# Kernel tuning notes

Hardware: AMD Instinct MI355X
Metric: run time of the kernel (lower is better)

The kernel has to match this reference:

```python
import jax, jax.numpy as jnp
import numpy as np


def conv1x1(x, W, b):
    # x: [B,C,H,W], W: [O,C] (1x1 conv kernel squeezed), b: [O]
    return jnp.einsum('bchw,oc->bohw', x, W) + b[None, :, None, None]


def setup_inputs() -> dict:
    key = jax.random.key(0)
    ks = jax.random.split(key, 16)
    B, C, H, W = 4, 2048, 32, 32
    HID = 256  # gate_strength_fc hidden width
    s = 1.0 / np.sqrt(C)
    x = jax.random.normal(ks[0], (B, C, H, W), dtype=jnp.float32)
    mask = jax.random.uniform(ks[1], (B, 1, H, W)) > 0.8
    use_entropy_gate = jax.random.randint(ks[2], (B,), 0, 2).astype(bool)
    return {
        'x': x,
        'Wq': jax.random.normal(ks[3], (C, C)) * s,
        'bq': jnp.zeros((C,), jnp.float32),
        'Wk': jax.random.normal(ks[4], (C, C)) * s,
        'bk': jnp.zeros((C,), jnp.float32),
        'Wv': jax.random.normal(ks[5], (C, C)) * s,
        'bv': jnp.zeros((C,), jnp.float32),
        'Wg': jax.random.normal(ks[6], (C, C)) * s,
        'bg': jnp.zeros((C,), jnp.float32),
        'W1': jax.random.normal(ks[7], (HID, C)) * s,
        'b1': jnp.zeros((HID,), jnp.float32),
        'W2': jax.random.normal(ks[8], (1, HID)) * (1.0 / np.sqrt(HID)),
        'b2': jnp.zeros((1,), jnp.float32),
        'mask': mask,
        'use_entropy_gate': use_entropy_gate,
    }


def reference(x, Wq, bq, Wk, bk, Wv, bv, Wg, bg, W1, b1, W2, b2, mask, use_entropy_gate):
    B, C, H, W = x.shape
    HW = H * W
    masked_x = x * mask.astype(x.dtype)
    # 1x1 conv projections, flattened over spatial dims
    q = conv1x1(masked_x, Wq, bq).reshape(B, C, HW).transpose(0, 2, 1)  # [B,HW,C]
    k = conv1x1(masked_x, Wk, bk).reshape(B, C, HW)                     # [B,C,HW]
    v = conv1x1(x, Wv, bv).reshape(B, C, HW)                            # [B,C,HW]
    # attention[b,n,m] = softmax_m(q[b,n,:] . k[b,:,m])
    attn = jax.nn.softmax(jnp.einsum('bnc,bcm->bnm', q, k), axis=-1)    # [B,HW,HW]
    # out = bmm(value, attention^T): out[b,c,m] = sum_n v[b,c,n] * attn[b,m,n]
    out = jnp.einsum('bcn,bmn->bcm', v, attn).reshape(B, C, H, W)
    # gate strength head: 2048 -> 256 -> 1, then sigmoid
    gate_strength = jax.nn.sigmoid(conv1x1(jax.nn.relu(conv1x1(x, W1, b1)), W2, b2))  # [B,1,H,W]
    gate = jax.nn.sigmoid(conv1x1(x, Wg, bg))                                          # [B,C,H,W]
    gated = out * gate * gate_strength
    # per-sample select: gated attention output where flag set, else passthrough x
    return jnp.where(use_entropy_gate[:, None, None, None], gated, x)
```

## Files before the change

kernel.cpp:

```cpp
#include <hip/hip_runtime.h>
#include <cstddef>
#include <cstdint>


typedef unsigned int u32;
typedef unsigned short u16;
typedef __attribute__((ext_vector_type(8))) short bf16x8;
typedef __attribute__((ext_vector_type(4))) float f32x4;

#define B_   4
#define C_   2048
#define HW_  1024
#define HID_ 256
#define KP   384
#define NQK  384
#define NVGH 1088

__device__ __forceinline__ float sigmoidf_(float x) {
  return 1.0f / (1.0f + __expf(-x));
}
__device__ __forceinline__ u16 f2bf(float f) {
  u32 u = __float_as_uint(f);
  return (u16)((u + 0x7FFFu + ((u >> 16) & 1u)) >> 16);
}
__device__ __forceinline__ float bf2f(u16 h) {
  return __uint_as_float(((u32)h) << 16);
}
__device__ __forceinline__ void gld16(void* lds, const void* g) {
  __builtin_amdgcn_global_load_lds(
      (const __attribute__((address_space(1))) u32*)g,
      (__attribute__((address_space(3))) u32*)lds, 16, 0, 0);
}

__device__ __forceinline__ void stage128x32s(u16* lds, const u16* g, int ld, int tid) {
#pragma unroll
  for (int t = 0; t < 2; ++t) {
    int s = tid + t * 256;
    int row = s >> 2;
    int oct = ((s & 3) - (row >> 1)) & 3;
    gld16(lds + (size_t)s * 8, g + (size_t)row * ld + oct * 8);
  }
}
template <int NF>
__device__ __forceinline__ void read_frags_s(const u16* lds, int base, int ln, int kq,
                                             bf16x8* f) {
#pragma unroll
  for (int t = 0; t < NF; ++t) {
    int row = base + t * 16 + ln;
    int oct = (kq + (row >> 1)) & 3;
    f[t] = *(const bf16x8*)(lds + (size_t)row * 32 + oct * 8);
  }
}

__global__ __launch_bounds__(256)
void scan_mask(const int* __restrict__ mask, int* __restrict__ idx,
               int* __restrict__ rnk, int* __restrict__ cnt)
{
  const int b = blockIdx.x;
  const int t = threadIdx.x;
  __shared__ int base;
  if (t == 0) base = 0;
  __syncthreads();
  int m0 = t * 4;
  int mv[4], local = 0;
#pragma unroll
  for (int i = 0; i < 4; ++i) { mv[i] = mask[b * HW_ + m0 + i] != 0; local += mv[i]; }
  int my = atomicAdd(&base, local);
#pragma unroll
  for (int i = 0; i < 4; ++i) {
    if (mv[i]) {
      int r = my++;
      if (r < KP) { idx[b * KP + r] = m0 + i; rnk[b * HW_ + m0 + i] = r; }
      else rnk[b * HW_ + m0 + i] = -1;
    } else {
      rnk[b * HW_ + m0 + i] = -1;
    }
  }
  __syncthreads();
  if (t == 0) cnt[b] = min(base, KP);
}

__global__ __launch_bounds__(256)
void transpose_fused(const float* __restrict__ x, u16* __restrict__ xhi,
                     u16* __restrict__ xkh, u16* __restrict__ xkl,
                     const int* __restrict__ rnk, const int* __restrict__ useg)
{
  const int b = blockIdx.z;
  if (!useg[b]) return;
  __shared__ float t[32][33];
  const int c0 = blockIdx.y * 32, j0 = blockIdx.x * 32;
  const int tid = threadIdx.x;
  const float* xb = x + ((size_t)b * C_ + c0) * (size_t)HW_ + j0;
  {
    int jj = tid & 31, cs = tid >> 5;
#pragma unroll
    for (int t4 = 0; t4 < 4; ++t4) {
      int c = cs * 4 + t4;
      t[c][jj] = xb[(size_t)c * HW_ + jj];
    }
  }
  __syncthreads();
  int j = tid >> 3, c4 = (tid & 7) * 4;
  float v0 = t[c4 + 0][j], v1 = t[c4 + 1][j], v2 = t[c4 + 2][j], v3 = t[c4 + 3][j];
  ushort4 hv;
  hv.x = f2bf(v0); hv.y = f2bf(v1); hv.z = f2bf(v2); hv.w = f2bf(v3);
  *(ushort4*)(xhi + ((size_t)b * HW_ + j0 + j) * (size_t)C_ + c0 + c4) = hv;
  int r = rnk[b * HW_ + j0 + j];
  if (r >= 0) {
    ushort4 lv;
    lv.x = f2bf(v0 - bf2f(hv.x)); lv.y = f2bf(v1 - bf2f(hv.y));
    lv.z = f2bf(v2 - bf2f(hv.z)); lv.w = f2bf(v3 - bf2f(hv.w));
    size_t o = ((size_t)b * KP + r) * (size_t)C_ + c0 + c4;
    *(ushort4*)(xkh + o) = hv;
    *(ushort4*)(xkl + o) = lv;
  }
}

__global__ __launch_bounds__(256)
void cast_all(const float* __restrict__ Wq, const float* __restrict__ Wk,
              const float* __restrict__ Wv, const float* __restrict__ Wg,
              const float* __restrict__ W1,
              u16* __restrict__ Wqkh, u16* __restrict__ Wqkl, u16* __restrict__ Wvgh)
{
  const int reg = blockIdx.y;
  int i = (blockIdx.x * 256 + threadIdx.x) * 4;
  const float* src; u16* dh; u16* dl = nullptr; int n = C_ * C_;
  if (reg == 0)      { src = Wq; dh = Wqkh;              dl = Wqkl; }
  else if (reg == 1) { src = Wk; dh = Wqkh + C_ * C_;    dl = Wqkl + C_ * C_; }
  else if (reg == 2) { src = Wv; dh = Wvgh; }
  else if (reg == 3) { src = Wg; dh = Wvgh + C_ * C_; }
  else               { src = W1; dh = Wvgh + 2 * C_ * C_; n = HID_ * C_; }
  if (i >= n) return;
  float4 v = *(const float4*)(src + i);
  ushort4 h;
  h.x = f2bf(v.x); h.y = f2bf(v.y); h.z = f2bf(v.z); h.w = f2bf(v.w);
  *(ushort4*)(dh + i) = h;
  if (dl) {
    ushort4 l;
    l.x = f2bf(v.x - bf2f(h.x)); l.y = f2bf(v.y - bf2f(h.y));
    l.z = f2bf(v.z - bf2f(h.z)); l.w = f2bf(v.w - bf2f(h.w));
    *(ushort4*)(dl + i) = l;
  }
}

__global__ __launch_bounds__(256, 2)
void mega2_proj(const u16* __restrict__ Wqkh, const u16* __restrict__ Wqkl,
                const u16* __restrict__ xkh, const u16* __restrict__ xkl,
                const u16* __restrict__ Wvgh, const u16* __restrict__ xhi,
                const float* __restrict__ bq, const float* __restrict__ bk,
                const float* __restrict__ bv, const float* __restrict__ bg,
                const float* __restrict__ b1,
                u16* __restrict__ qTh, u16* __restrict__ qTl,
                u16* __restrict__ kTh, u16* __restrict__ kTl,
                u16* __restrict__ vk2, float* __restrict__ sv,
                u16* __restrict__ gate, float* __restrict__ h,
                const int* __restrict__ rnk,
                const int* __restrict__ cnt, const int* __restrict__ useg)
{
  __shared__ u16 lds[4 * 128 * 32];
  const int tid = threadIdx.x;
  const int w = tid >> 6, lane = tid & 63, ln = lane & 15, kq = lane >> 4;
  const int bid = blockIdx.x;

  if (bid < NQK) {
    const int b = bid & 3;
    if (!useg[b]) return;
    const int rest = bid >> 2;
    const int row0 = (rest / 3) * 128;
    const int col0 = (rest % 3) * 128;
    const int RC = (cnt[b] + 127) & ~127;
    if (col0 >= RC) return;
    u16* Ah = lds; u16* Al = lds + 4096; u16* Bh = lds + 8192; u16* Bl = lds + 12288;
    const int wm = (w >> 1) * 64, wn = (w & 1) * 64;
    f32x4 acc[4][4];
#pragma unroll
    for (int i = 0; i < 4; ++i)
#pragma unroll
      for (int j = 0; j < 4; ++j) acc[i][j] = (f32x4){0.f, 0.f, 0.f, 0.f};

    const u16* Ahb = Wqkh + (size_t)row0 * C_;
    const u16* Alb = Wqkl + (size_t)row0 * C_;
    const u16* Bhb = xkh + ((size_t)b * KP + col0) * (size_t)C_;
    const u16* Blb = xkl + ((size_t)b * KP + col0) * (size_t)C_;

    for (int k0 = 0; k0 < C_; k0 += 32) {
      __syncthreads();
      stage128x32s(Ah, Ahb + k0, C_, tid);
      stage128x32s(Al, Alb + k0, C_, tid);
      stage128x32s(Bh, Bhb + k0, C_, tid);
      stage128x32s(Bl, Blb + k0, C_, tid);
      __syncthreads();
      bf16x8 ah[4], al[4], bh[4], bl[4];
      read_frags_s<4>(Ah, wm, ln, kq, ah);
      read_frags_s<4>(Al, wm, ln, kq, al);
      read_frags_s<4>(Bh, wn, ln, kq, bh);
      read_frags_s<4>(Bl, wn, ln, kq, bl);
#pragma unroll
      for (int i = 0; i < 4; ++i)
#pragma unroll
        for (int j = 0; j < 4; ++j) {
          acc[i][j] = __builtin_amdgcn_mfma_f32_16x16x32_bf16(ah[i], bh[j], acc[i][j], 0, 0, 0);
          acc[i][j] = __builtin_amdgcn_mfma_f32_16x16x32_bf16(ah[i], bl[j], acc[i][j], 0, 0, 0);
          acc[i][j] = __builtin_amdgcn_mfma_f32_16x16x32_bf16(al[i], bh[j], acc[i][j], 0, 0, 0);
        }
    }

    const int half = row0 >= C_;
    const float* bias = half ? bk : bq;
    u16* Oh = half ? kTh : qTh;
    u16* Ol = half ? kTl : qTl;
    const int mbase = row0 - (half ? C_ : 0);
#pragma unroll
    for (int i = 0; i < 4; ++i) {
      int m = mbase + wm + i * 16 + kq * 4;
      float b4[4];
#pragma unroll
      for (int r = 0; r < 4; ++r) b4[r] = bias[m + r];
#pragma unroll
      for (int j = 0; j < 4; ++j) {
        int n = col0 + wn + j * 16 + ln;
        float v0 = acc[i][j][0] + b4[0];
        float v1 = acc[i][j][1] + b4[1];
        float v2 = acc[i][j][2] + b4[2];
        float v3 = acc[i][j][3] + b4[3];
        ushort4 hv, lv;
        hv.x = f2bf(v0); lv.x = f2bf(v0 - bf2f(hv.x));
        hv.y = f2bf(v1); lv.y = f2bf(v1 - bf2f(hv.y));
        hv.z = f2bf(v2); lv.z = f2bf(v2 - bf2f(hv.z));
        hv.w = f2bf(v3); lv.w = f2bf(v3 - bf2f(hv.w));
        size_t o = ((size_t)b * KP + n) * (size_t)C_ + m;
        *(ushort4*)(Oh + o) = hv;
        *(ushort4*)(Ol + o) = lv;
      }
    }
  } else {
    const int bid2 = bid - NQK;
    const int col = bid2 & 7;
    const int b = (bid2 >> 3) & 3;
    const int row0 = (bid2 >> 5) * 128;
    if (!useg[b]) return;
    const int pix0 = col * 128;
    u16* As = lds;
    u16* Bs = lds + 4096;
    const int wm = (w >> 1) * 64, wn = (w & 1) * 64;
    f32x4 acc[4][4];
#pragma unroll
    for (int i = 0; i < 4; ++i)
#pragma unroll
      for (int j = 0; j < 4; ++j) acc[i][j] = (f32x4){0.f, 0.f, 0.f, 0.f};

    const u16* Ab = Wvgh + (size_t)row0 * C_;
    const u16* Bb = xhi + ((size_t)b * HW_ + pix0) * (size_t)C_;

    for (int k0 = 0; k0 < C_; k0 += 32) {
      __syncthreads();
      stage128x32s(As, Ab + k0, C_, tid);
      stage128x32s(Bs, Bb + k0, C_, tid);
      __syncthreads();
      bf16x8 af[4], bf[4];
      read_frags_s<4>(As, wm, ln, kq, af);
      read_frags_s<4>(Bs, wn, ln, kq, bf);
#pragma unroll
      for (int i = 0; i < 4; ++i)
#pragma unroll
        for (int j = 0; j < 4; ++j)
          acc[i][j] = __builtin_amdgcn_mfma_f32_16x16x32_bf16(af[i], bf[j], acc[i][j], 0, 0, 0);
    }

    const int sect = (row0 >= 2 * C_) ? 2 : (row0 >= C_ ? 1 : 0);
    const float* bias = (sect == 0) ? bv : (sect == 1 ? bg : b1);
    const int sbase = (sect == 0) ? 0 : (sect == 1 ? C_ : 2 * C_);
#pragma unroll
    for (int i = 0; i < 4; ++i) {
      int ml = row0 - sbase + wm + i * 16 + kq * 4;
      float b4[4];
#pragma unroll
      for (int r = 0; r < 4; ++r) b4[r] = bias[ml + r];
      float srow[4] = {0.f, 0.f, 0.f, 0.f};
#pragma unroll
      for (int j = 0; j < 4; ++j) {
        int pp = pix0 + wn + j * 16 + ln;
        int rv = (sect == 0) ? rnk[b * HW_ + pp] : 0;
#pragma unroll
        for (int r = 0; r < 4; ++r) {
          float val = acc[i][j][r] + b4[r];
          if (sect == 0) {
            srow[r] += val;
            if (rv >= 0) vk2[((size_t)b * C_ + ml + r) * (size_t)KP + rv] = f2bf(val);
          } else if (sect == 1) {
            gate[((size_t)b * C_ + ml + r) * (size_t)HW_ + pp] = f2bf(sigmoidf_(val));
          } else {
            h[((size_t)b * HID_ + ml + r) * (size_t)HW_ + pp] = fmaxf(val, 0.f);
          }
        }
      }
      if (sect == 0) {
#pragma unroll
        for (int r = 0; r < 4; ++r) {
          float s = srow[r];
          s += __shfl_down(s, 8);
          s += __shfl_down(s, 4);
          s += __shfl_down(s, 2);
          s += __shfl_down(s, 1);
          if (ln == 0) atomicAdd(&sv[(size_t)b * C_ + ml + r], s);
        }
      }
    }
  }
}

__global__ __launch_bounds__(256, 2)
void logits_splitk(const u16* __restrict__ qTh, const u16* __restrict__ qTl,
                   const u16* __restrict__ kTh, const u16* __restrict__ kTl,
                   float* __restrict__ lk, const int* __restrict__ cnt,
                   const int* __restrict__ useg)
{
  const int b = blockIdx.z >> 3, ks = blockIdx.z & 7;
  if (!useg[b]) return;
  const int RC = (cnt[b] + 127) & ~127;
  const int row0 = blockIdx.y * 128, col0 = blockIdx.x * 128;
  if (row0 >= RC || col0 >= RC) return;
  __shared__ u16 lds[4 * 128 * 32];
  u16* Ah = lds; u16* Al = lds + 4096; u16* Bh = lds + 8192; u16* Bl = lds + 12288;
  const int tid = threadIdx.x;
  const int w = tid >> 6, lane = tid & 63, ln = lane & 15, kq = lane >> 4;
  const int wm = (w >> 1) * 64, wn = (w & 1) * 64;
  f32x4 acc[4][4];
#pragma unroll
  for (int i = 0; i < 4; ++i)
#pragma unroll
    for (int j = 0; j < 4; ++j) acc[i][j] = (f32x4){0.f, 0.f, 0.f, 0.f};

  const size_t bs = (size_t)b * KP * (size_t)C_;
  const u16* Ahb = qTh + bs + (size_t)row0 * C_;
  const u16* Alb = qTl + bs + (size_t)row0 * C_;
  const u16* Bhb = kTh + bs + (size_t)col0 * C_;
  const u16* Blb = kTl + bs + (size_t)col0 * C_;
  const int kbeg = ks * 256, kend = kbeg + 256;

  for (int k0 = kbeg; k0 < kend; k0 += 32) {
    __syncthreads();
    stage128x32s(Ah, Ahb + k0, C_, tid);
    stage128x32s(Al, Alb + k0, C_, tid);
    stage128x32s(Bh, Bhb + k0, C_, tid);
    stage128x32s(Bl, Blb + k0, C_, tid);
    __syncthreads();
    bf16x8 ah[4], al[4], bh[4], bl[4];
    read_frags_s<4>(Ah, wm, ln, kq, ah);
    read_frags_s<4>(Al, wm, ln, kq, al);
    read_frags_s<4>(Bh, wn, ln, kq, bh);
    read_frags_s<4>(Bl, wn, ln, kq, bl);
#pragma unroll
    for (int i = 0; i < 4; ++i)
#pragma unroll
      for (int j = 0; j < 4; ++j) {
        acc[i][j] = __builtin_amdgcn_mfma_f32_16x16x32_bf16(ah[i], bh[j], acc[i][j], 0, 0, 0);
        acc[i][j] = __builtin_amdgcn_mfma_f32_16x16x32_bf16(ah[i], bl[j], acc[i][j], 0, 0, 0);
        acc[i][j] = __builtin_amdgcn_mfma_f32_16x16x32_bf16(al[i], bh[j], acc[i][j], 0, 0, 0);
      }
  }

#pragma unroll
  for (int i = 0; i < 4; ++i) {
    int m = row0 + wm + i * 16 + kq * 4;
#pragma unroll
    for (int j = 0; j < 4; ++j) {
      int n = col0 + wn + j * 16 + ln;
#pragma unroll
      for (int r = 0; r < 4; ++r)
        atomicAdd(&lk[((size_t)b * KP + m + r) * (size_t)KP + n], acc[i][j][r]);
    }
  }
}

__global__ __launch_bounds__(256)
void softmax_ind(const float* __restrict__ lk, const int* __restrict__ rnk,
                 const int* __restrict__ cnt, const int* __restrict__ useg,
                 u16* __restrict__ attn_k, float* __restrict__ cm)
{
  const int b = blockIdx.y;
  if (!useg[b]) return;
  const int mo = blockIdx.x;
  const int t = threadIdx.x;
  const int r = rnk[b * HW_ + mo];
  if (r < 0) {
    if (t == 0) cm[b * HW_ + mo] = 1.0f / HW_;
    return;
  }
  const int n = cnt[b];
  const float* row = lk + ((size_t)b * KP + r) * (size_t)KP;
  float v0 = -1e30f, v1 = -1e30f;
  if (t < n) v0 = row[t];
  if (t + 256 < n) v1 = row[t + 256];

  float mx = fmaxf(fmaxf(v0, v1), 0.0f);
#pragma unroll
  for (int off = 32; off > 0; off >>= 1) mx = fmaxf(mx, __shfl_down(mx, off));
  __shared__ float red[8];
  const int wid = t >> 6;
  if ((t & 63) == 0) red[wid] = mx;
  __syncthreads();
  if (t == 0) red[4] = fmaxf(fmaxf(red[0], red[1]), fmaxf(red[2], red[3]));
  __syncthreads();
  mx = red[4];

  float e0 = (t < n) ? __expf(v0 - mx) : 0.f;
  float e1 = (t + 256 < n) ? __expf(v1 - mx) : 0.f;
  float s = e0 + e1;
#pragma unroll
  for (int off = 32; off > 0; off >>= 1) s += __shfl_down(s, off);
  if ((t & 63) == 0) red[wid] = s;
  __syncthreads();
  if (t == 0) red[5] = red[0] + red[1] + red[2] + red[3] + (HW_ - n) * __expf(-mx);
  __syncthreads();
  float inv = 1.0f / red[5];
  float c = __expf(-mx) * inv;
  if (t == 0) cm[b * HW_ + mo] = c;

  u16* arow = attn_k + ((size_t)b * HW_ + mo) * (size_t)KP;
  if (t < n) arow[t] = f2bf(e0 * inv - c);
  if (t + 256 < n) arow[t + 256] = f2bf(e1 * inv - c);
}

__global__ __launch_bounds__(256)
void gate_strength_k(const float* __restrict__ h, const float* __restrict__ W2,
                     const float* __restrict__ b2, float* __restrict__ gs,
                     const int* __restrict__ useg)
{
  const int b = blockIdx.x >> 4;
  if (!useg[b]) return;
  const int tid = threadIdx.x;
  const int jc = (blockIdx.x & 15) * 64;
  const int j = jc + (tid & 63), is = tid >> 6;
  const float* hb = h + (size_t)b * HID_ * HW_;
  float s = 0.f;
  for (int i = is; i < HID_; i += 4) s = fmaf(W2[i], hb[(size_t)i * HW_ + j], s);
  __shared__ float red[4][64];
  red[is][tid & 63] = s;
  __syncthreads();
  if (is == 0) {
    float tot = red[0][tid] + red[1][tid] + red[2][tid] + red[3][tid];
    gs[(size_t)b * HW_ + j] = sigmoidf_(tot + b2[0]);
  }
}

__global__ __launch_bounds__(256, 2)
void out_compact(const u16* __restrict__ vk2, const u16* __restrict__ attn_k,
                 const float* __restrict__ cm, const float* __restrict__ sv,
                 const u16* __restrict__ gate, const float* __restrict__ gs,
                 const float* __restrict__ x, const int* __restrict__ cnt,
                 const int* __restrict__ useg, float* __restrict__ Out)
{
  const int b = blockIdx.z;
  const int tid = threadIdx.x;
  const int row0 = blockIdx.y * 128, col0 = blockIdx.x * 128;
  if (!useg[b]) {
    const float* xb = x + ((size_t)b * C_ + row0) * (size_t)HW_ + col0;
    float* ob = Out + ((size_t)b * C_ + row0) * (size_t)HW_ + col0;
#pragma unroll
    for (int t = 0; t < 16; ++t) {
      int i2 = tid + t * 256;
      int r = i2 >> 5, c4 = (i2 & 31) * 4;
      *(float4*)(ob + (size_t)r * HW_ + c4) = *(const float4*)(xb + (size_t)r * HW_ + c4);
    }
    return;
  }
  __shared__ u16 lds[2 * 128 * 32];
  u16* As = lds; u16* Bs = lds + 4096;
  const int w = tid >> 6, lane = tid & 63, ln = lane & 15, kq = lane >> 4;
  const int wm = (w >> 1) * 64, wn = (w & 1) * 64;
  f32x4 acc[4][4];
#pragma unroll
  for (int i = 0; i < 4; ++i)
#pragma unroll
    for (int j = 0; j < 4; ++j) acc[i][j] = (f32x4){0.f, 0.f, 0.f, 0.f};

  const int KR = (cnt[b] + 31) & ~31;
  const u16* Ab = vk2 + ((size_t)b * C_ + row0) * (size_t)KP;
  const u16* Bb = attn_k + ((size_t)b * HW_ + col0) * (size_t)KP;

  for (int k0 = 0; k0 < KR; k0 += 32) {
    __syncthreads();
    stage128x32s(As, Ab + k0, KP, tid);
    stage128x32s(Bs, Bb + k0, KP, tid);
    __syncthreads();
    bf16x8 af[4], bf[4];
    read_frags_s<4>(As, wm, ln, kq, af);
    read_frags_s<4>(Bs, wn, ln, kq, bf);
#pragma unroll
    for (int i = 0; i < 4; ++i)
#pragma unroll
      for (int j = 0; j < 4; ++j)
        acc[i][j] = __builtin_amdgcn_mfma_f32_16x16x32_bf16(af[i], bf[j], acc[i][j], 0, 0, 0);
  }

#pragma unroll
  for (int i = 0; i < 4; ++i) {
    int c = row0 + wm + i * 16 + kq * 4;
    float sv4[4];
#pragma unroll
    for (int r = 0; r < 4; ++r) sv4[r] = sv[(size_t)b * C_ + c + r];
#pragma unroll
    for (int j = 0; j < 4; ++j) {
      int m = col0 + wn + j * 16 + ln;
      float cmv = cm[(size_t)b * HW_ + m];
      float gsv = gs[(size_t)b * HW_ + m];
#pragma unroll
      for (int r = 0; r < 4; ++r) {
        size_t off = ((size_t)b * C_ + c + r) * (size_t)HW_ + m;
        float val = acc[i][j][r] + cmv * sv4[r];
        Out[off] = val * bf2f(gate[off]) * gsv;
      }
    }
  }
}

extern "C" void kernel_launch(void* const* d_in, const int* in_sizes, int n_in,
                              void* d_out, int out_size, void* d_ws, size_t ws_size,
                              hipStream_t stream)
{
  (void)in_sizes; (void)n_in; (void)out_size; (void)ws_size;

  const float* x  = (const float*)d_in[0];
  const float* Wq = (const float*)d_in[1];
  const float* bq = (const float*)d_in[2];
  const float* Wk = (const float*)d_in[3];
  const float* bk = (const float*)d_in[4];
  const float* Wv = (const float*)d_in[5];
  const float* bv = (const float*)d_in[6];
  const float* Wg = (const float*)d_in[7];
  const float* bg = (const float*)d_in[8];
  const float* W1 = (const float*)d_in[9];
  const float* b1 = (const float*)d_in[10];
  const float* W2 = (const float*)d_in[11];
  const float* b2 = (const float*)d_in[12];
  const int* mask = (const int*)d_in[13];
  const int* useg = (const int*)d_in[14];
  float* out = (float*)d_out;

  char* p = (char*)d_ws;
  const size_t SZ_T  = (size_t)B_ * HW_ * C_ * sizeof(u16);
  const size_t SZ_W  = (size_t)2 * C_ * C_ * sizeof(u16);
  const size_t SZ_VG = ((size_t)2 * C_ + HID_) * C_ * sizeof(u16);
  const size_t SZ_XK = (size_t)B_ * KP * C_ * sizeof(u16);

  u16* xhi  = (u16*)p; p += SZ_T;
  u16* Wqkh = (u16*)p; p += SZ_W;
  u16* Wqkl = (u16*)p; p += SZ_W;
  u16* Wvgh = (u16*)p; p += SZ_VG;
  u16* xkh  = (u16*)p; p += SZ_XK;
  u16* xkl  = (u16*)p; p += SZ_XK;
  u16* qTh  = (u16*)p; p += SZ_XK;
  u16* qTl  = (u16*)p; p += SZ_XK;
  u16* kTh  = (u16*)p; p += SZ_XK;
  u16* kTl  = (u16*)p; p += SZ_XK;
  u16* gate = (u16*)p; p += SZ_T;
  u16* vk2  = (u16*)p; p += (size_t)B_ * C_ * KP * sizeof(u16);
  float* h  = (float*)p; p += (size_t)B_ * HID_ * HW_ * sizeof(float);
  float* cm = (float*)p; p += (size_t)B_ * HW_ * sizeof(float);
  float* sv = (float*)p; p += (size_t)B_ * C_ * sizeof(float);
  float* gs = (float*)p; p += (size_t)B_ * HW_ * sizeof(float);
  int* idx = (int*)p; p += (size_t)B_ * KP * sizeof(int);
  int* rnk = (int*)p; p += (size_t)B_ * HW_ * sizeof(int);
  int* cnt = (int*)p; p += 64;

  float* lk     = (float*)Wqkh;
  u16*   attn_k = (u16*)((char*)Wqkh + (size_t)B_ * KP * KP * 4);

  dim3 blk(256);

  scan_mask<<<dim3(B_), blk, 0, stream>>>(mask, idx, rnk, cnt);
  hipMemsetAsync(xkh, 0, SZ_XK, stream);
  hipMemsetAsync(xkl, 0, SZ_XK, stream);
  hipMemsetAsync(vk2, 0, (size_t)B_ * C_ * KP * sizeof(u16), stream);
  hipMemsetAsync(sv, 0, (size_t)B_ * C_ * sizeof(float), stream);
  transpose_fused<<<dim3(HW_ / 32, C_ / 32, B_), blk, 0, stream>>>(
      x, xhi, xkh, xkl, rnk, useg);
  cast_all<<<dim3(4096, 5), blk, 0, stream>>>(Wq, Wk, Wv, Wg, W1, Wqkh, Wqkl, Wvgh);

  mega2_proj<<<dim3(NQK + NVGH), blk, 0, stream>>>(
      Wqkh, Wqkl, xkh, xkl, Wvgh, xhi, bq, bk, bv, bg, b1,
      qTh, qTl, kTh, kTl, vk2, sv, gate, h, rnk, cnt, useg);

  hipMemsetAsync(lk, 0, (size_t)B_ * KP * KP * sizeof(float), stream);
  hipMemsetAsync(attn_k, 0, (size_t)B_ * HW_ * KP * sizeof(u16), stream);

  logits_splitk<<<dim3(KP / 128, KP / 128, B_ * 8), blk, 0, stream>>>(
      qTh, qTl, kTh, kTl, lk, cnt, useg);

  softmax_ind<<<dim3(HW_, B_), blk, 0, stream>>>(lk, rnk, cnt, useg, attn_k, cm);

  gate_strength_k<<<dim3(B_ * 16), blk, 0, stream>>>(h, W2, b2, gs, useg);

  out_compact<<<dim3(HW_ / 128, C_ / 128, B_), blk, 0, stream>>>(
      vk2, attn_k, cm, sv, gate, gs, x, cnt, useg, out);
}
```

Measured before the change: 395.5 us.

## Double-buffer LDS staging in all GEMM kernels to overlap loads with MFMA

Converts the single-buffer stage/sync/compute loops in the projection, QK-logit and output GEMM kernels into a ping-pong double-buffered pipeline. The next K tile is staged into the alternate LDS buffer while MFMAs run on the current one, removing one barrier per step and hiding global-load latency. It doubles LDS use per block (64KB for the QK paths), which may reduce occupancy below the launch-bounds target of 2 blocks/CU. The output kernel handles an odd tile count with a tail compute.

```diff
diff --git a/kernel.cpp b/kernel.cpp
--- a/kernel.cpp
+++ b/kernel.cpp
@@ -50,6 +50,46 @@
     int oct = (kq + (row >> 1)) & 3;
     f[t] = *(const bf16x8*)(lds + (size_t)row * 32 + oct * 8);
   }
+}
+
+__device__ __forceinline__ void stage_qk4(u16* L, const u16* Ah, const u16* Al,
+                                          const u16* Bh, const u16* Bl, int k0, int tid) {
+  stage128x32s(L,         Ah + k0, C_, tid);
+  stage128x32s(L + 4096,  Al + k0, C_, tid);
+  stage128x32s(L + 8192,  Bh + k0, C_, tid);
+  stage128x32s(L + 12288, Bl + k0, C_, tid);
+}
+__device__ __forceinline__ void stage_ab2(u16* L, const u16* A, const u16* Bp, int k0,
+                                          int lda, int ldb, int tid) {
+  stage128x32s(L,        A + k0, lda, tid);
+  stage128x32s(L + 4096, Bp + k0, ldb, tid);
+}
+__device__ __forceinline__ void comp_qk(const u16* L, int wm, int wn, int ln, int kq,
+                                        f32x4 (&acc)[4][4]) {
+  bf16x8 ah[4], al[4], bh[4], bl[4];
+  read_frags_s<4>(L, wm, ln, kq, ah);
+  read_frags_s<4>(L + 4096, wm, ln, kq, al);
+  read_frags_s<4>(L + 8192, wn, ln, kq, bh);
+  read_frags_s<4>(L + 12288, wn, ln, kq, bl);
+#pragma unroll
+  for (int i = 0; i < 4; ++i)
+#pragma unroll
+    for (int j = 0; j < 4; ++j) {
+      acc[i][j] = __builtin_amdgcn_mfma_f32_16x16x32_bf16(ah[i], bh[j], acc[i][j], 0, 0, 0);
+      acc[i][j] = __builtin_amdgcn_mfma_f32_16x16x32_bf16(ah[i], bl[j], acc[i][j], 0, 0, 0);
+      acc[i][j] = __builtin_amdgcn_mfma_f32_16x16x32_bf16(al[i], bh[j], acc[i][j], 0, 0, 0);
+    }
+}
+__device__ __forceinline__ void comp_ab(const u16* L, int wm, int wn, int ln, int kq,
+                                        f32x4 (&acc)[4][4]) {
+  bf16x8 af[4], bg_[4];
+  read_frags_s<4>(L, wm, ln, kq, af);
+  read_frags_s<4>(L + 4096, wn, ln, kq, bg_);
+#pragma unroll
+  for (int i = 0; i < 4; ++i)
+#pragma unroll
+    for (int j = 0; j < 4; ++j)
+      acc[i][j] = __builtin_amdgcn_mfma_f32_16x16x32_bf16(af[i], bg_[j], acc[i][j], 0, 0, 0);
 }
 
 __global__ __launch_bounds__(256)
@@ -157,7 +197,8 @@
                 const int* __restrict__ rnk,
                 const int* __restrict__ cnt, const int* __restrict__ useg)
 {
-  __shared__ u16 lds[4 * 128 * 32];
+  __shared__ u16 lds0[4 * 4096];
+  __shared__ u16 lds1[4 * 4096];
   const int tid = threadIdx.x;
   const int w = tid >> 6, lane = tid & 63, ln = lane & 15, kq = lane >> 4;
   const int bid = blockIdx.x;
@@ -170,7 +211,6 @@
     const int col0 = (rest % 3) * 128;
     const int RC = (cnt[b] + 127) & ~127;
     if (col0 >= RC) return;
-    u16* Ah = lds; u16* Al = lds + 4096; u16* Bh = lds + 8192; u16* Bl = lds + 12288;
     const int wm = (w >> 1) * 64, wn = (w & 1) * 64;
     f32x4 acc[4][4];
 #pragma unroll
@@ -183,26 +223,15 @@
     const u16* Bhb = xkh + ((size_t)b * KP + col0) * (size_t)C_;
     const u16* Blb = xkl + ((size_t)b * KP + col0) * (size_t)C_;
 
-    for (int k0 = 0; k0 < C_; k0 += 32) {
+    stage_qk4(lds0, Ahb, Alb, Bhb, Blb, 0, tid);
+    __syncthreads();
+    for (int t = 0; t < 64; t += 2) {
+      stage_qk4(lds1, Ahb, Alb, Bhb, Blb, (t + 1) * 32, tid);
+      comp_qk(lds0, wm, wn, ln, kq, acc);
       __syncthreads();
-      stage128x32s(Ah, Ahb + k0, C_, tid);
-      stage128x32s(Al, Alb + k0, C_, tid);
-      stage128x32s(Bh, Bhb + k0, C_, tid);
-      stage128x32s(Bl, Blb + k0, C_, tid);
+      if (t + 2 < 64) stage_qk4(lds0, Ahb, Alb, Bhb, Blb, (t + 2) * 32, tid);
+      comp_qk(lds1, wm, wn, ln, kq, acc);
       __syncthreads();
-      bf16x8 ah[4], al[4], bh[4], bl[4];
-      read_frags_s<4>(Ah, wm, ln, kq, ah);
-      read_frags_s<4>(Al, wm, ln, kq, al);
-      read_frags_s<4>(Bh, wn, ln, kq, bh);
-      read_frags_s<4>(Bl, wn, ln, kq, bl);
-#pragma unroll
-      for (int i = 0; i < 4; ++i)
-#pragma unroll
-        for (int j = 0; j < 4; ++j) {
-          acc[i][j] = __builtin_amdgcn_mfma_f32_16x16x32_bf16(ah[i], bh[j], acc[i][j], 0, 0, 0);
-          acc[i][j] = __builtin_amdgcn_mfma_f32_16x16x32_bf16(ah[i], bl[j], acc[i][j], 0, 0, 0);
-          acc[i][j] = __builtin_amdgcn_mfma_f32_16x16x32_bf16(al[i], bh[j], acc[i][j], 0, 0, 0);
-        }
     }
 
     const int half = row0 >= C_;
@@ -240,8 +269,6 @@
     const int row0 = (bid2 >> 5) * 128;
     if (!useg[b]) return;
     const int pix0 = col * 128;
-    u16* As = lds;
-    u16* Bs = lds + 4096;
     const int wm = (w >> 1) * 64, wn = (w & 1) * 64;
     f32x4 acc[4][4];
 #pragma unroll
@@ -252,19 +279,15 @@
     const u16* Ab = Wvgh + (size_t)row0 * C_;
     const u16* Bb = xhi + ((size_t)b * HW_ + pix0) * (size_t)C_;
 
-    for (int k0 = 0; k0 < C_; k0 += 32) {
+    stage_ab2(lds0, Ab, Bb, 0, C_, C_, tid);
+    __syncthreads();
+    for (int t = 0; t < 64; t += 2) {
+      stage_ab2(lds1, Ab, Bb, (t + 1) * 32, C_, C_, tid);
+      comp_ab(lds0, wm, wn, ln, kq, acc);
       __syncthreads();
-      stage128x32s(As, Ab + k0, C_, tid);
-      stage128x32s(Bs, Bb + k0, C_, tid);
+      if (t + 2 < 64) stage_ab2(lds0, Ab, Bb, (t + 2) * 32, C_, C_, tid);
+      comp_ab(lds1, wm, wn, ln, kq, acc);
       __syncthreads();
-      bf16x8 af[4], bf[4];
-      read_frags_s<4>(As, wm, ln, kq, af);
-      read_frags_s<4>(Bs, wn, ln, kq, bf);
-#pragma unroll
-      for (int i = 0; i < 4; ++i)
-#pragma unroll
-        for (int j = 0; j < 4; ++j)
-          acc[i][j] = __builtin_amdgcn_mfma_f32_16x16x32_bf16(af[i], bf[j], acc[i][j], 0, 0, 0);
     }
 
     const int sect = (row0 >= 2 * C_) ? 2 : (row0 >= C_ ? 1 : 0);
@@ -320,8 +343,8 @@
   const int RC = (cnt[b] + 127) & ~127;
   const int row0 = blockIdx.y * 128, col0 = blockIdx.x * 128;
   if (row0 >= RC || col0 >= RC) return;
-  __shared__ u16 lds[4 * 128 * 32];
-  u16* Ah = lds; u16* Al = lds + 4096; u16* Bh = lds + 8192; u16* Bl = lds + 12288;
+  __shared__ u16 lds0[4 * 4096];
+  __shared__ u16 lds1[4 * 4096];
   const int tid = threadIdx.x;
   const int w = tid >> 6, lane = tid & 63, ln = lane & 15, kq = lane >> 4;
   const int wm = (w >> 1) * 64, wn = (w & 1) * 64;
@@ -336,28 +359,17 @@
   const u16* Alb = qTl + bs + (size_t)row0 * C_;
   const u16* Bhb = kTh + bs + (size_t)col0 * C_;
   const u16* Blb = kTl + bs + (size_t)col0 * C_;
-  const int kbeg = ks * 256, kend = kbeg + 256;
-
-  for (int k0 = kbeg; k0 < kend; k0 += 32) {
+  const int kbeg = ks * 256;
+
+  stage_qk4(lds0, Ahb, Alb, Bhb, Blb, kbeg, tid);
+  __syncthreads();
+  for (int t = 0; t < 8; t += 2) {
+    stage_qk4(lds1, Ahb, Alb, Bhb, Blb, kbeg + (t + 1) * 32, tid);
+    comp_qk(lds0, wm, wn, ln, kq, acc);
     __syncthreads();
-    stage128x32s(Ah, Ahb + k0, C_, tid);
-    stage128x32s(Al, Alb + k0, C_, tid);
-    stage128x32s(Bh, Bhb + k0, C_, tid);
-    stage128x32s(Bl, Blb + k0, C_, tid);
+    if (t + 2 < 8) stage_qk4(lds0, Ahb, Alb, Bhb, Blb, kbeg + (t + 2) * 32, tid);
+    comp_qk(lds1, wm, wn, ln, kq, acc);
     __syncthreads();
-    bf16x8 ah[4], al[4], bh[4], bl[4];
-    read_frags_s<4>(Ah, wm, ln, kq, ah);
-    read_frags_s<4>(Al, wm, ln, kq, al);
-    read_frags_s<4>(Bh, wn, ln, kq, bh);
-    read_frags_s<4>(Bl, wn, ln, kq, bl);
-#pragma unroll
-    for (int i = 0; i < 4; ++i)
-#pragma unroll
-      for (int j = 0; j < 4; ++j) {
-        acc[i][j] = __builtin_amdgcn_mfma_f32_16x16x32_bf16(ah[i], bh[j], acc[i][j], 0, 0, 0);
-        acc[i][j] = __builtin_amdgcn_mfma_f32_16x16x32_bf16(ah[i], bl[j], acc[i][j], 0, 0, 0);
-        acc[i][j] = __builtin_amdgcn_mfma_f32_16x16x32_bf16(al[i], bh[j], acc[i][j], 0, 0, 0);
-      }
   }
 
 #pragma unroll
@@ -465,8 +477,8 @@
     }
     return;
   }
-  __shared__ u16 lds[2 * 128 * 32];
-  u16* As = lds; u16* Bs = lds + 4096;
+  __shared__ u16 lds0[2 * 4096];
+  __shared__ u16 lds1[2 * 4096];
   const int w = tid >> 6, lane = tid & 63, ln = lane & 15, kq = lane >> 4;
   const int wm = (w >> 1) * 64, wn = (w & 1) * 64;
   f32x4 acc[4][4];
@@ -476,23 +488,22 @@
     for (int j = 0; j < 4; ++j) acc[i][j] = (f32x4){0.f, 0.f, 0.f, 0.f};
 
   const int KR = (cnt[b] + 31) & ~31;
+  const int NT = KR / 32;
   const u16* Ab = vk2 + ((size_t)b * C_ + row0) * (size_t)KP;
   const u16* Bb = attn_k + ((size_t)b * HW_ + col0) * (size_t)KP;
 
-  for (int k0 = 0; k0 < KR; k0 += 32) {
+  stage_ab2(lds0, Ab, Bb, 0, KP, KP, tid);
+  __syncthreads();
+  int t = 0;
+  for (; t + 2 <= NT; t += 2) {
+    stage_ab2(lds1, Ab, Bb, (t + 1) * 32, KP, KP, tid);
+    comp_ab(lds0, wm, wn, ln, kq, acc);
     __syncthreads();
-    stage128x32s(As, Ab + k0, KP, tid);
-    stage128x32s(Bs, Bb + k0, KP, tid);
+    if (t + 2 < NT) stage_ab2(lds0, Ab, Bb, (t + 2) * 32, KP, KP, tid);
+    comp_ab(lds1, wm, wn, ln, kq, acc);
     __syncthreads();
-    bf16x8 af[4], bf[4];
-    read_frags_s<4>(As, wm, ln, kq, af);
-    read_frags_s<4>(Bs, wn, ln, kq, bf);
-#pragma unroll
-    for (int i = 0; i < 4; ++i)
-#pragma unroll
-      for (int j = 0; j < 4; ++j)
-        acc[i][j] = __builtin_amdgcn_mfma_f32_16x16x32_bf16(af[i], bf[j], acc[i][j], 0, 0, 0);
-  }
+  }
+  if (t < NT) comp_ab(lds0, wm, wn, ln, kq, acc);
 
 #pragma unroll
   for (int i = 0; i < 4; ++i) {
```

Result: slower. 407.6 us (+3.1%).
